# Kernel tuning notes

Hardware: AMD Instinct MI355X
Metric: run time of the kernel (lower is better)

The kernel has to match this reference:

```python
import jax, jax.numpy as jnp
import numpy as np

N = 100000   # nodes
E = 400000   # edges per relation
K = 2        # n_hop relations
D = 256      # in_dim
ATT = 64     # att_dim
L = 3        # n_layer
H1, H2 = 128, 64
EPS = 1e-5
NEG_SLOPE = 0.01


def setup_inputs() -> dict:
    key = jax.random.key(0)
    ks = jax.random.split(key, 16)
    s = 1.0 / np.sqrt(D)
    return {
        "x": jax.random.normal(ks[0], (N, D), jnp.float32),
        "edges_index": jax.random.randint(ks[1], (K, 2, E), 0, N),
        "edges_weight": jax.random.uniform(ks[2], (K, E), jnp.float32),
        "bn_gamma": jnp.ones((D,), jnp.float32),
        "bn_beta": jnp.zeros((D,), jnp.float32),
        "gcn_W": jax.random.normal(ks[3], (L, D, D), jnp.float32) * s,
        "gcn_b": jnp.zeros((L, D), jnp.float32),
        "att_lin_W": jax.random.normal(ks[4], (L, K, D, ATT), jnp.float32) * s,
        "att_lin_b": jnp.zeros((L, K, ATT), jnp.float32),
        "att_q": jax.random.normal(ks[5], (L, K, ATT), jnp.float32) * (1.0 / np.sqrt(ATT)),
        "proj_W1": jax.random.normal(ks[6], (D, H1), jnp.float32) * s,
        "proj_b1": jnp.zeros((H1,), jnp.float32),
        "proj_W2": jax.random.normal(ks[7], (H1, H2), jnp.float32) * (1.0 / np.sqrt(H1)),
        "proj_b2": jnp.zeros((H2,), jnp.float32),
    }


def _gcn_aggregate(row, col, w, xw):
    # symmetric gcn_norm on adj_t (add_self_loops=False):
    # deg[i] = sum of w over edges with col == i
    deg = jax.ops.segment_sum(w, col, num_segments=N)
    dinv = jnp.where(deg > 0, 1.0 / jnp.sqrt(deg), 0.0)
    norm = dinv[col] * w * dinv[row]                       # [E]
    # out[c] += norm * xw[r]
    return jax.ops.segment_sum(norm[:, None] * xw[row], col, num_segments=N)


def reference(x, edges_index, edges_weight, bn_gamma, bn_beta, gcn_W, gcn_b,
              att_lin_W, att_lin_b, att_q, proj_W1, proj_b1, proj_W2, proj_b2):
    # BatchNorm1d (training-mode batch stats)
    mu = jnp.mean(x, axis=0)
    var = jnp.mean((x - mu) ** 2, axis=0)
    h = (x - mu) / jnp.sqrt(var + EPS) * bn_gamma + bn_beta   # [N, D]

    rows = edges_index[:, 0, :]  # [K, E]
    cols = edges_index[:, 1, :]

    for i in range(L):
        xw = h @ gcn_W[i]                                     # shared transform [N, D]
        # per-relation sparse aggregation, vmapped over K
        xs = jax.vmap(_gcn_aggregate, in_axes=(0, 0, 0, None))(
            rows, cols, edges_weight, xw) + gcn_b[i]          # [K, N, D]
        # HanAtt: softmax over hops of per-node scores
        keys = jnp.tanh(jnp.einsum('knd,kdh->knh', xs, att_lin_W[i]) + att_lin_b[i][:, None, :])
        sim = jnp.einsum('knh,kh->kn', keys, att_q[i])        # [K, N]
        alpha = jax.nn.softmax(sim, axis=0)                   # softmax over K
        h = jnp.einsum('knd,kn->nd', xs, alpha)               # [N, D]
        h = jax.nn.relu(h)

    h = jax.nn.leaky_relu(h @ proj_W1 + proj_b1, NEG_SLOPE)
    h = jax.nn.leaky_relu(h @ proj_W2 + proj_b2, NEG_SLOPE)
    return h
```

## Files before the change

kernel.cpp:

```cpp
#include <hip/hip_runtime.h>
#include <hip/hip_bf16.h>
#include <math.h>

#define NN 100000
#define EE 400000
#define KD 2
#define DD 256
#define ATTD 64
#define LL 3
#define HH1 128
#define HH2 64
#define EPSV 1e-5f
#define SLOPE 0.01f
#define KN (KD * NN)
#define WFP 33554432.0f

typedef short short8 __attribute__((ext_vector_type(8)));
typedef float floatx4 __attribute__((ext_vector_type(4)));
typedef unsigned int u32x4 __attribute__((ext_vector_type(4)));
typedef unsigned short u16;
typedef unsigned int u32;
typedef unsigned long long u64;

__device__ __forceinline__ u16 f2bf(float f) {
    u32 u = __float_as_uint(f);
    return (u16)((u + 0x7fffu + ((u >> 16) & 1u)) >> 16);
}
__device__ __forceinline__ float bf2f(u16 h) {
    return __uint_as_float((u32)h << 16);
}

__device__ __forceinline__ void fma_row8_(float4& a0, float4& a1, uint4 w, float nv) {
    float2 f0 = __bfloat1622float2(*(const __hip_bfloat162*)&w.x);
    float2 f1 = __bfloat1622float2(*(const __hip_bfloat162*)&w.y);
    float2 f2 = __bfloat1622float2(*(const __hip_bfloat162*)&w.z);
    float2 f3 = __bfloat1622float2(*(const __hip_bfloat162*)&w.w);
    a0.x += nv * f0.x; a0.y += nv * f0.y; a0.z += nv * f1.x; a0.w += nv * f1.y;
    a1.x += nv * f2.x; a1.y += nv * f2.y; a1.z += nv * f3.x; a1.w += nv * f3.y;
}

__global__ void bn_stats(const float* __restrict__ x, float* __restrict__ sums) {
    int d = threadIdx.x;
    int r0 = blockIdx.x * 125;
    float s = 0.f, sq = 0.f;
    for (int r = r0; r < r0 + 125; ++r) {
        float v = x[(size_t)r * DD + d];
        s += v; sq += v * v;
    }
    atomicAdd(&sums[d], s);
    atomicAdd(&sums[DD + d], sq);
}

__global__ void bn_apply(const float* __restrict__ x, const float* __restrict__ sums,
                         const float* __restrict__ gamma, const float* __restrict__ beta,
                         u16* __restrict__ h_hi, u16* __restrict__ h_lo) {
    size_t i = (size_t)blockIdx.x * blockDim.x + threadIdx.x;
    const float inv_n = 1.f / NN;
    int dq = (int)(i & 63) * 4;
    float4 xv = ((const float4*)x)[i];
    ushort4 hv, lv;
    float* xp = (float*)&xv;
    u16* hp = (u16*)&hv; u16* lp = (u16*)&lv;
#pragma unroll
    for (int j = 0; j < 4; ++j) {
        int d = dq + j;
        float mu = sums[d] * inv_n;
        float var = sums[DD + d] * inv_n - mu * mu;
        float inv = rsqrtf(var + EPSV);
        float v = (xp[j] - mu) * inv * gamma[d] + beta[d];
        u16 hb = f2bf(v);
        hp[j] = hb;
        lp[j] = f2bf(v - bf2f(hb));
    }
    ((ushort4*)h_hi)[i] = hv;
    ((ushort4*)h_lo)[i] = lv;
}

__global__ void deg_count(const int* __restrict__ ei, const float* __restrict__ w,
                          u64* __restrict__ dc) {
    int i = blockIdx.x * blockDim.x + threadIdx.x;
    if (i >= KD * EE) return;
    int k = i / EE, e = i - k * EE;
    int col = ei[(size_t)k * 2 * EE + EE + e];
    u64 wfp = (u64)__float2uint_rn(w[i] * WFP);
    atomicAdd(&dc[k * NN + col], ((u64)1 << 32) | wfp);
}

__global__ void dinv_pack(const u64* __restrict__ dc, float* __restrict__ dinv,
                          int* __restrict__ starts) {
    int i = blockIdx.x * blockDim.x + threadIdx.x;
    if (i >= KN) return;
    u64 p = dc[i];
    float deg = (float)(u32)p * (1.f / WFP);
    dinv[i] = deg > 0.f ? 1.f / sqrtf(deg) : 0.f;
    starts[i] = (int)(p >> 32);
}

#define SCAN_NB ((KN + 255) / 256)
__global__ void scan_blocks(int* __restrict__ starts, int* __restrict__ bsums) {
    __shared__ int tmp[256];
    int t = threadIdx.x;
    int idx = blockIdx.x * 256 + t;
    int v = (idx < KN) ? starts[idx] : 0;
    tmp[t] = v;
    __syncthreads();
#pragma unroll
    for (int off = 1; off < 256; off <<= 1) {
        int s = (t >= off) ? tmp[t - off] : 0;
        __syncthreads();
        tmp[t] += s;
        __syncthreads();
    }
    if (idx < KN) starts[idx] = tmp[t] - v;
    if (t == 255) bsums[blockIdx.x] = tmp[255];
}

__global__ void scan_sums(int* __restrict__ bsums) {
    __shared__ int tmp[1024];
    int t = threadIdx.x;
    int v = (t < SCAN_NB) ? bsums[t] : 0;
    tmp[t] = v;
    __syncthreads();
#pragma unroll
    for (int off = 1; off < 1024; off <<= 1) {
        int s = (t >= off) ? tmp[t - off] : 0;
        __syncthreads();
        tmp[t] += s;
        __syncthreads();
    }
    if (t < SCAN_NB) bsums[t] = tmp[t] - v;
}

__global__ void scan_add(int* __restrict__ starts, const int* __restrict__ bsums) {
    int idx = blockIdx.x * 256 + threadIdx.x;
    if (idx < KN) starts[idx] += bsums[blockIdx.x];
}

__global__ void csr_fill(const int* __restrict__ ei, const float* __restrict__ w,
                         const float* __restrict__ dinv,
                         int* __restrict__ starts, int2* __restrict__ edata) {
    int i = blockIdx.x * blockDim.x + threadIdx.x;
    if (i >= KD * EE) return;
    int k = i / EE, e = i - k * EE;
    const int* eik = ei + (size_t)k * 2 * EE;
    int row = eik[e], col = eik[EE + e];
    float nv = dinv[k * NN + col] * w[i] * dinv[k * NN + row];
    int pos = atomicAdd(&starts[k * NN + col], 1);
    edata[pos] = make_int2(row, __float_as_int(nv));
}

#define GCN_T (LL * DD * DD)
#define ATT_T (LL * KD * DD * ATTD)
#define P1_T  (DD * HH1)
#define P2_T  (HH1 * HH2)
#define WC_TOTAL (GCN_T + ATT_T + P1_T + P2_T)
__device__ __forceinline__ void wconv1(const float* __restrict__ W, u16* __restrict__ Wt,
                                       int i, int Kd, int Nc) {
    int kk = i / Nc, n = i - kk * Nc;
    Wt[(size_t)n * Kd + kk] = f2bf(W[i]);
}
__global__ void wconv_all(const float* __restrict__ gcnW, u16* __restrict__ gcnWb,
                          const float* __restrict__ attW, u16* __restrict__ attWb,
                          const float* __restrict__ pW1, u16* __restrict__ pW1b,
                          const float* __restrict__ pW2, u16* __restrict__ pW2b) {
    int gid = blockIdx.x * 256 + threadIdx.x;
    if (gid >= WC_TOTAL) return;
    if (gid < GCN_T) {
        int l = gid >> 16, i = gid & 65535;
        wconv1(gcnW + (size_t)l * DD * DD, gcnWb + (size_t)l * DD * DD, i, DD, DD);
    } else if (gid < GCN_T + ATT_T) {
        int g = gid - GCN_T;
        int lk = g >> 14, i = g & 16383;
        wconv1(attW + (size_t)lk * DD * ATTD, attWb + (size_t)lk * ATTD * DD, i, DD, ATTD);
    } else if (gid < GCN_T + ATT_T + P1_T) {
        wconv1(pW1, pW1b, gid - (GCN_T + ATT_T), DD, HH1);
    } else {
        wconv1(pW2, pW2b, gid - (GCN_T + ATT_T + P1_T), HH1, HH2);
    }
}

__global__ void att_bias_fold(const float* __restrict__ attW, const float* __restrict__ attb,
                              const float* __restrict__ gcnb, float* __restrict__ batt) {
    int lk = blockIdx.x;
    int a = threadIdx.x;
    int l = lk >> 1;
    const float* W = attW + (size_t)lk * DD * ATTD;
    const float* gb = gcnb + l * DD;
    float s = attb[lk * ATTD + a];
    for (int d = 0; d < DD; ++d) s += gb[d] * W[d * ATTD + a];
    batt[lk * ATTD + a] = s;
}

#define LDSP 40

template<int BN_, int MODE, bool PRESPLIT, bool BIAS, int ACT>
__global__ __launch_bounds__(256) void gemm_mfma(
        const float* __restrict__ A,
        const u16* __restrict__ Ahi, const u16* __restrict__ Alo,
        const u16* __restrict__ Bt, const float* __restrict__ bias,
        float* __restrict__ Cf, u16* __restrict__ Cb,
        int M, int Kd, int Nc) {
    constexpr int JW = BN_ / 64;
    __shared__ u16 AsHi[64 * LDSP];
    __shared__ u16 AsLo[64 * LDSP];
    __shared__ u16 Bs[BN_ * LDSP];

    const int tid = threadIdx.x;
    const int lane = tid & 63, wx = tid >> 6;
    const int lane15 = lane & 15, quad = lane >> 4;
    const int bm = blockIdx.x * 64;
    const int bn = blockIdx.y * BN_;

    floatx4 acc[4][JW];
#pragma unroll
    for (int i = 0; i < 4; ++i)
#pragma unroll
        for (int j = 0; j < JW; ++j) acc[i][j] = (floatx4){0.f, 0.f, 0.f, 0.f};

    for (int k0 = 0; k0 < Kd; k0 += 32) {
        if constexpr (PRESPLIT) {
            {
                int m = tid >> 2, ko = (tid & 3) << 3;
                uint4 vh = make_uint4(0, 0, 0, 0), vl = make_uint4(0, 0, 0, 0);
                if (bm + m < M) {
                    vh = *(const uint4*)(Ahi + (size_t)(bm + m) * Kd + k0 + ko);
                    vl = *(const uint4*)(Alo + (size_t)(bm + m) * Kd + k0 + ko);
                }
                *(uint4*)(void*)(AsHi + m * LDSP + ko) = vh;
                *(uint4*)(void*)(AsLo + m * LDSP + ko) = vl;
            }
        } else {
#pragma unroll
            for (int t = tid; t < 512; t += 256) {
                int m = t >> 3, k4 = (t & 7) << 2;
                float4 v = make_float4(0.f, 0.f, 0.f, 0.f);
                if (bm + m < M) v = *(const float4*)(A + (size_t)(bm + m) * Kd + k0 + k4);
                u16 h0 = f2bf(v.x), h1 = f2bf(v.y), h2 = f2bf(v.z), h3 = f2bf(v.w);
                *(ushort4*)(void*)(AsHi + m * LDSP + k4) = make_ushort4(h0, h1, h2, h3);
                u16 l0 = f2bf(v.x - bf2f(h0)), l1 = f2bf(v.y - bf2f(h1));
                u16 l2 = f2bf(v.z - bf2f(h2)), l3 = f2bf(v.w - bf2f(h3));
                *(ushort4*)(void*)(AsLo + m * LDSP + k4) = make_ushort4(l0, l1, l2, l3);
            }
        }
#pragma unroll
        for (int t = tid; t < BN_ * 4; t += 256) {
            int n = t >> 2, ko = (t & 3) << 3;
            uint4 w = *(const uint4*)(Bt + (size_t)(bn + n) * Kd + k0 + ko);
            *(uint4*)(void*)(Bs + n * LDSP + ko) = w;
        }
        __syncthreads();

        const u16* pA  = AsHi + lane15 * LDSP + quad * 8;
        const u16* pAl = AsLo + lane15 * LDSP + quad * 8;
        const u16* pB  = Bs + (wx * (BN_ / 4) + lane15) * LDSP + quad * 8;
        short8 b[JW];
#pragma unroll
        for (int j = 0; j < JW; ++j) b[j] = *(const short8*)(pB + j * 16 * LDSP);
#pragma unroll
        for (int i = 0; i < 4; ++i) {
            short8 a = *(const short8*)(pA + i * 16 * LDSP);
#pragma unroll
            for (int j = 0; j < JW; ++j)
                acc[i][j] = __builtin_amdgcn_mfma_f32_16x16x32_bf16(a, b[j], acc[i][j], 0, 0, 0);
        }
#pragma unroll
        for (int i = 0; i < 4; ++i) {
            short8 a = *(const short8*)(pAl + i * 16 * LDSP);
#pragma unroll
            for (int j = 0; j < JW; ++j)
                acc[i][j] = __builtin_amdgcn_mfma_f32_16x16x32_bf16(a, b[j], acc[i][j], 0, 0, 0);
        }
        __syncthreads();
    }

#pragma unroll
    for (int i = 0; i < 4; ++i) {
#pragma unroll
        for (int r = 0; r < 4; ++r) {
            int row = bm + i * 16 + quad * 4 + r;
            if (row >= M) continue;
#pragma unroll
            for (int j = 0; j < JW; ++j) {
                int col = bn + wx * (BN_ / 4) + j * 16 + lane15;
                float v = acc[i][j][r];
                if constexpr (BIAS) v += bias[col];
                if constexpr (ACT == 1) v = v > 0.f ? v : SLOPE * v;
                if constexpr (MODE == 0) Cf[(size_t)row * Nc + col] = v;
                else                     Cb[(size_t)row * Nc + col] = f2bf(v);
            }
        }
    }
}

#define BMF 32
#define ALDS 264

__global__ __launch_bounds__(256) void att_fused(
        const int* __restrict__ starts, const int2* __restrict__ edata,
        const u16* __restrict__ xw, const u16* __restrict__ Bt,
        const float* __restrict__ batt, const float* __restrict__ qv,
        const float* __restrict__ gcnb,
        u16* __restrict__ h_hi, u16* __restrict__ h_lo) {
    __shared__ u16 As[KD * BMF * ALDS];
    __shared__ float simbuf[KD][2][BMF];

    const int tid = threadIdx.x;
    const int lane = tid & 63, waveid = tid >> 6;
    const int l32 = tid & 31;
    const int hid = tid >> 5;
    const int base = lane & 32;
    const int bm = blockIdx.x * BMF;

    {
        const int kk = hid >> 2;
        const int r0 = (hid & 3) * 8;
        const int widx0 = kk * NN + bm + r0;
        int sv = 0;
        if (l32 < 9) {
            int idx = widx0 - 1 + l32;
            sv = idx >= 0 ? starts[idx] : 0;
        }
        int2 ed[8];
#pragma unroll
        for (int g = 0; g < 8; ++g) {
            int b = __shfl(sv, base + g), e = __shfl(sv, base + g + 1);
            ed[g] = (l32 < e - b) ? edata[b + l32] : make_int2(0, 0);
        }
#pragma unroll
        for (int g = 0; g < 8; g += 2) {
            int bA = __shfl(sv, base + g),     eA = __shfl(sv, base + g + 1);
            int eB = __shfl(sv, base + g + 2);
            int bB = eA;
            int dA = eA - bA, dB = eB - bB;
            int mA = dA > 32 ? 32 : dA, mB = dB > 32 ? 32 : dB;
            float4 xa0 = make_float4(0.f,0.f,0.f,0.f), xa1 = make_float4(0.f,0.f,0.f,0.f);
            float4 xb0 = make_float4(0.f,0.f,0.f,0.f), xb1 = make_float4(0.f,0.f,0.f,0.f);
            int j = 0;
            for (; j + 4 <= mA && j + 4 <= mB; j += 4) {
                int ra0 = __shfl(ed[g].x, base + j),     ra1 = __shfl(ed[g].x, base + j + 1);
                int ra2 = __shfl(ed[g].x, base + j + 2), ra3 = __shfl(ed[g].x, base + j + 3);
                int rb0 = __shfl(ed[g+1].x, base + j),     rb1 = __shfl(ed[g+1].x, base + j + 1);
                int rb2 = __shfl(ed[g+1].x, base + j + 2), rb3 = __shfl(ed[g+1].x, base + j + 3);
                float na0 = __int_as_float(__shfl(ed[g].y, base + j));
                float na1 = __int_as_float(__shfl(ed[g].y, base + j + 1));
                float na2 = __int_as_float(__shfl(ed[g].y, base + j + 2));
                float na3 = __int_as_float(__shfl(ed[g].y, base + j + 3));
                float nb0 = __int_as_float(__shfl(ed[g+1].y, base + j));
                float nb1 = __int_as_float(__shfl(ed[g+1].y, base + j + 1));
                float nb2 = __int_as_float(__shfl(ed[g+1].y, base + j + 2));
                float nb3 = __int_as_float(__shfl(ed[g+1].y, base + j + 3));
                uint4 wa0 = *(const uint4*)(xw + (size_t)ra0 * DD + l32 * 8);
                uint4 wa1 = *(const uint4*)(xw + (size_t)ra1 * DD + l32 * 8);
                uint4 wa2 = *(const uint4*)(xw + (size_t)ra2 * DD + l32 * 8);
                uint4 wa3 = *(const uint4*)(xw + (size_t)ra3 * DD + l32 * 8);
                uint4 wb0 = *(const uint4*)(xw + (size_t)rb0 * DD + l32 * 8);
                uint4 wb1 = *(const uint4*)(xw + (size_t)rb1 * DD + l32 * 8);
                uint4 wb2 = *(const uint4*)(xw + (size_t)rb2 * DD + l32 * 8);
                uint4 wb3 = *(const uint4*)(xw + (size_t)rb3 * DD + l32 * 8);
                fma_row8_(xa0, xa1, wa0, na0);
                fma_row8_(xa0, xa1, wa1, na1);
                fma_row8_(xa0, xa1, wa2, na2);
                fma_row8_(xa0, xa1, wa3, na3);
                fma_row8_(xb0, xb1, wb0, nb0);
                fma_row8_(xb0, xb1, wb1, nb1);
                fma_row8_(xb0, xb1, wb2, nb2);
                fma_row8_(xb0, xb1, wb3, nb3);
            }
            int jb = j;
            for (; j + 4 <= mA; j += 4) {
                int ra0 = __shfl(ed[g].x, base + j),     ra1 = __shfl(ed[g].x, base + j + 1);
                int ra2 = __shfl(ed[g].x, base + j + 2), ra3 = __shfl(ed[g].x, base + j + 3);
                float na0 = __int_as_float(__shfl(ed[g].y, base + j));
                float na1 = __int_as_float(__shfl(ed[g].y, base + j + 1));
                float na2 = __int_as_float(__shfl(ed[g].y, base + j + 2));
                float na3 = __int_as_float(__shfl(ed[g].y, base + j + 3));
                uint4 wa0 = *(const uint4*)(xw + (size_t)ra0 * DD + l32 * 8);
                uint4 wa1 = *(const uint4*)(xw + (size_t)ra1 * DD + l32 * 8);
                uint4 wa2 = *(const uint4*)(xw + (size_t)ra2 * DD + l32 * 8);
                uint4 wa3 = *(const uint4*)(xw + (size_t)ra3 * DD + l32 * 8);
                fma_row8_(xa0, xa1, wa0, na0);
                fma_row8_(xa0, xa1, wa1, na1);
                fma_row8_(xa0, xa1, wa2, na2);
                fma_row8_(xa0, xa1, wa3, na3);
            }
            for (; j < mA; ++j) {
                int r = __shfl(ed[g].x, base + j);
                float nv = __int_as_float(__shfl(ed[g].y, base + j));
                uint4 w = *(const uint4*)(xw + (size_t)r * DD + l32 * 8);
                fma_row8_(xa0, xa1, w, nv);
            }
            for (; jb + 4 <= mB; jb += 4) {
                int rb0 = __shfl(ed[g+1].x, base + jb),     rb1 = __shfl(ed[g+1].x, base + jb + 1);
                int rb2 = __shfl(ed[g+1].x, base + jb + 2), rb3 = __shfl(ed[g+1].x, base + jb + 3);
                float nb0 = __int_as_float(__shfl(ed[g+1].y, base + jb));
                float nb1 = __int_as_float(__shfl(ed[g+1].y, base + jb + 1));
                float nb2 = __int_as_float(__shfl(ed[g+1].y, base + jb + 2));
                float nb3 = __int_as_float(__shfl(ed[g+1].y, base + jb + 3));
                uint4 wb0 = *(const uint4*)(xw + (size_t)rb0 * DD + l32 * 8);
                uint4 wb1 = *(const uint4*)(xw + (size_t)rb1 * DD + l32 * 8);
                uint4 wb2 = *(const uint4*)(xw + (size_t)rb2 * DD + l32 * 8);
                uint4 wb3 = *(const uint4*)(xw + (size_t)rb3 * DD + l32 * 8);
                fma_row8_(xb0, xb1, wb0, nb0);
                fma_row8_(xb0, xb1, wb1, nb1);
                fma_row8_(xb0, xb1, wb2, nb2);
                fma_row8_(xb0, xb1, wb3, nb3);
            }
            for (; jb < mB; ++jb) {
                int r = __shfl(ed[g+1].x, base + jb);
                float nv = __int_as_float(__shfl(ed[g+1].y, base + jb));
                uint4 w = *(const uint4*)(xw + (size_t)r * DD + l32 * 8);
                fma_row8_(xb0, xb1, w, nv);
            }
            for (int e2 = bA + 32; e2 < eA; ++e2) {
                int2 ee = edata[e2];
                float nv = __int_as_float(ee.y);
                uint4 w = *(const uint4*)(xw + (size_t)ee.x * DD + l32 * 8);
                fma_row8_(xa0, xa1, w, nv);
            }
            for (int e2 = bB + 32; e2 < eB; ++e2) {
                int2 ee = edata[e2];
                float nv = __int_as_float(ee.y);
                uint4 w = *(const uint4*)(xw + (size_t)ee.x * DD + l32 * 8);
                fma_row8_(xb0, xb1, w, nv);
            }
            u32x4 st;
            st.x = (u32)f2bf(xa0.x) | ((u32)f2bf(xa0.y) << 16);
            st.y = (u32)f2bf(xa0.z) | ((u32)f2bf(xa0.w) << 16);
            st.z = (u32)f2bf(xa1.x) | ((u32)f2bf(xa1.y) << 16);
            st.w = (u32)f2bf(xa1.z) | ((u32)f2bf(xa1.w) << 16);
            *(u32x4*)(void*)(As + (kk * BMF + r0 + g) * ALDS + l32 * 8) = st;
            st.x = (u32)f2bf(xb0.x) | ((u32)f2bf(xb0.y) << 16);
            st.y = (u32)f2bf(xb0.z) | ((u32)f2bf(xb0.w) << 16);
            st.z = (u32)f2bf(xb1.x) | ((u32)f2bf(xb1.y) << 16);
            st.w = (u32)f2bf(xb1.z) | ((u32)f2bf(xb1.w) << 16);
            *(u32x4*)(void*)(As + (kk * BMF + r0 + g + 1) * ALDS + l32 * 8) = st;
        }
    }
    __syncthreads();

    const int kw = waveid >> 1, ch = waveid & 1;
    const int lane15 = lane & 15, quad = lane >> 4;
    floatx4 acc[2][2];
#pragma unroll
    for (int i = 0; i < 2; ++i)
#pragma unroll
        for (int j = 0; j < 2; ++j) acc[i][j] = (floatx4){0.f, 0.f, 0.f, 0.f};

    const u16* pB0 = Bt + (size_t)kw * ATTD * DD + (size_t)(ch * 32 + lane15) * DD + quad * 8;
    const u16* pB1 = pB0 + 16 * DD;
#pragma unroll
    for (int k0 = 0; k0 < DD; k0 += 32) {
        short8 b0 = *(const short8*)(pB0 + k0);
        short8 b1 = *(const short8*)(pB1 + k0);
        const u16* pA = As + (kw * BMF + lane15) * ALDS + k0 + quad * 8;
#pragma unroll
        for (int i = 0; i < 2; ++i) {
            short8 a = *(const short8*)(pA + i * 16 * ALDS);
            acc[i][0] = __builtin_amdgcn_mfma_f32_16x16x32_bf16(a, b0, acc[i][0], 0, 0, 0);
            acc[i][1] = __builtin_amdgcn_mfma_f32_16x16x32_bf16(a, b1, acc[i][1], 0, 0, 0);
        }
    }

#pragma unroll
    for (int i = 0; i < 2; ++i) {
#pragma unroll
        for (int r = 0; r < 4; ++r) {
            float p = 0.f;
#pragma unroll
            for (int j = 0; j < 2; ++j) {
                int col = ch * 32 + j * 16 + lane15;
                float v = acc[i][j][r] + batt[kw * ATTD + col];
                float ex = __expf(2.f * v);
                float th = 1.f - 2.f / (ex + 1.f);
                p += th * qv[kw * ATTD + col];
            }
            p += __shfl_xor(p, 1, 64);
            p += __shfl_xor(p, 2, 64);
            p += __shfl_xor(p, 4, 64);
            p += __shfl_xor(p, 8, 64);
            if (lane15 == 0) simbuf[kw][ch][i * 16 + quad * 4 + r] = p;
        }
    }
    __syncthreads();

#pragma unroll
    for (int it = 0; it < 4; ++it) {
        int item = tid + it * 256;
        int row = item >> 5, c8 = item & 31;
        int grow = bm + row;
        float s0 = simbuf[0][0][row] + simbuf[0][1][row];
        float s1 = simbuf[1][0][row] + simbuf[1][1][row];
        float m = fmaxf(s0, s1);
        float e0 = __expf(s0 - m), e1 = __expf(s1 - m);
        float inv = 1.f / (e0 + e1);
        float a0 = e0 * inv, a1 = e1 * inv;
        uint4 x0 = *(const uint4*)(As + row * ALDS + c8 * 8);
        uint4 x1 = *(const uint4*)(As + (BMF + row) * ALDS + c8 * 8);
        const float* bp = gcnb + c8 * 8;
        uint4 hiw, low;
        u16* hp = (u16*)&hiw; u16* lp = (u16*)&low;
        const u32* xp0 = (const u32*)&x0; const u32* xp1 = (const u32*)&x1;
#pragma unroll
        for (int j = 0; j < 4; ++j) {
            float2 f0 = __bfloat1622float2(*(const __hip_bfloat162*)&xp0[j]);
            float2 f1 = __bfloat1622float2(*(const __hip_bfloat162*)&xp1[j]);
            float ra = fmaxf(0.f, a0 * f0.x + a1 * f1.x + bp[2 * j]);
            float rb = fmaxf(0.f, a0 * f0.y + a1 * f1.y + bp[2 * j + 1]);
            u16 ha = f2bf(ra), hb = f2bf(rb);
            hp[2 * j] = ha; hp[2 * j + 1] = hb;
            lp[2 * j] = f2bf(ra - bf2f(ha));
            lp[2 * j + 1] = f2bf(rb - bf2f(hb));
        }
        *(uint4*)(h_hi + (size_t)grow * DD + c8 * 8) = hiw;
        *(uint4*)(h_lo + (size_t)grow * DD + c8 * 8) = low;
    }
}

extern "C" void kernel_launch(void* const* d_in, const int* in_sizes, int n_in,
                              void* d_out, int out_size, void* d_ws, size_t ws_size,
                              hipStream_t stream) {
    const float* x     = (const float*)d_in[0];
    const int*   ei    = (const int*)d_in[1];
    const float* ew    = (const float*)d_in[2];
    const float* gamma = (const float*)d_in[3];
    const float* beta  = (const float*)d_in[4];
    const float* gcn_W = (const float*)d_in[5];
    const float* gcn_b = (const float*)d_in[6];
    const float* att_W = (const float*)d_in[7];
    const float* att_b = (const float*)d_in[8];
    const float* att_q = (const float*)d_in[9];
    const float* pW1   = (const float*)d_in[10];
    const float* pb1   = (const float*)d_in[11];
    const float* pW2   = (const float*)d_in[12];
    const float* pb2   = (const float*)d_in[13];
    float* out = (float*)d_out;

    char* wsb = (char*)d_ws;
    size_t off = 0;
    auto alloc = [&](size_t bytes) -> void* {
        void* p = wsb + off;
        off += (bytes + 255) & ~(size_t)255;
        return p;
    };
    u16*   h_hi  = (u16*)alloc((size_t)NN * DD * 2);
    u16*   h_lo  = (u16*)alloc((size_t)NN * DD * 2);
    u16*   xw    = (u16*)alloc((size_t)NN * DD * 2);
    float* p1tmp = (float*)xw;
    float* dinv  = (float*)alloc((size_t)KN * 4);
    int*   starts= (int*)alloc(((size_t)KN + 1) * 4);
    u64*   dc    = (u64*)alloc((size_t)KN * 8);
    int2*  edata = (int2*)alloc((size_t)KD * EE * 8);
    float* bnsums= (float*)alloc(2 * DD * 4);
    u16*   gcnWb = (u16*)alloc((size_t)LL * DD * DD * 2);
    u16*   attWb = (u16*)alloc((size_t)LL * KD * ATTD * DD * 2);
    u16*   pW1b  = (u16*)alloc((size_t)HH1 * DD * 2);
    u16*   pW2b  = (u16*)alloc((size_t)HH2 * HH1 * 2);
    float* batt  = (float*)alloc((size_t)LL * KD * ATTD * 4);
    int*   bsums = (int*)alloc((size_t)SCAN_NB * 4);

    wconv_all<<<(WC_TOTAL + 255) / 256, 256, 0, stream>>>(
        gcn_W, gcnWb, att_W, attWb, pW1, pW1b, pW2, pW2b);
    att_bias_fold<<<LL * KD, ATTD, 0, stream>>>(att_W, att_b, gcn_b, batt);

    hipMemsetAsync(bnsums, 0, 2 * DD * 4, stream);
    bn_stats<<<800, 256, 0, stream>>>(x, bnsums);
    bn_apply<<<25000, 256, 0, stream>>>(x, bnsums, gamma, beta, h_hi, h_lo);

    hipMemsetAsync(dc, 0, (size_t)KN * 8, stream);
    deg_count<<<(KD * EE + 255) / 256, 256, 0, stream>>>(ei, ew, dc);
    dinv_pack<<<(KN + 255) / 256, 256, 0, stream>>>(dc, dinv, starts);
    scan_blocks<<<SCAN_NB, 256, 0, stream>>>(starts, bsums);
    scan_sums<<<1, 1024, 0, stream>>>(bsums);
    scan_add<<<SCAN_NB, 256, 0, stream>>>(starts, bsums);
    csr_fill<<<(KD * EE + 255) / 256, 256, 0, stream>>>(ei, ew, dinv, starts, edata);

    const int MB64 = (NN + 63) / 64;
    const int MBF  = NN / BMF;
    for (int l = 0; l < LL; ++l) {
        gemm_mfma<256, 1, true, false, 0><<<dim3(MB64, 1), 256, 0, stream>>>(
            nullptr, h_hi, h_lo, gcnWb + (size_t)l * DD * DD, nullptr,
            nullptr, xw, NN, DD, DD);
        att_fused<<<MBF, 256, 0, stream>>>(
            starts, edata, xw, attWb + (size_t)l * KD * ATTD * DD,
            batt + (size_t)l * KD * ATTD, att_q + (size_t)l * KD * ATTD,
            gcn_b + l * DD, h_hi, h_lo);
    }

    gemm_mfma<128, 0, true, true, 1><<<dim3(MB64, 1), 256, 0, stream>>>(
        nullptr, h_hi, h_lo, pW1b, pb1, p1tmp, nullptr, NN, DD, HH1);
    gemm_mfma<64, 0, false, true, 1><<<dim3(MB64, 1), 256, 0, stream>>>(
        p1tmp, nullptr, nullptr, pW2b, pb2, out, nullptr, NN, HH1, HH2);
}
```

Baseline: 904.7 us.

## Fuse next layer's GCN weight GEMM into attention aggregation kernel epilogue

For the first two layers, the fused aggregation/attention kernel now keeps the post-ReLU h tile (hi/lo bf16 split) in shared memory. It multiplies that tile by the next layer's GCN weight with MFMA and writes xw directly into a ping-pong buffer. This removes two standalone GEMM launches and the global write and re-read of h_hi/h_lo between layers. In exchange, each 32-row block re-reads the full 256x256 weight from global/L2, adds register pressure, and writes xw with scalar 2-byte stores.

```diff
diff --git a/kernel.cpp b/kernel.cpp
--- a/kernel.cpp
+++ b/kernel.cpp
@@ -295,11 +295,13 @@
 #define BMF 32
 #define ALDS 264
 
+template<bool LAST>
 __global__ __launch_bounds__(256) void att_fused(
         const int* __restrict__ starts, const int2* __restrict__ edata,
         const u16* __restrict__ xw, const u16* __restrict__ Bt,
         const float* __restrict__ batt, const float* __restrict__ qv,
         const float* __restrict__ gcnb,
+        const u16* __restrict__ Wnext, u16* __restrict__ xwout,
         u16* __restrict__ h_hi, u16* __restrict__ h_lo) {
     __shared__ u16 As[KD * BMF * ALDS];
     __shared__ float simbuf[KD][2][BMF];
@@ -314,7 +316,8 @@
     {
         const int kk = hid >> 2;
         const int r0 = (hid & 3) * 8;
-        const int widx0 = kk * NN + bm + r0;
+        const int widx0 = kk * NN + bm + (hid & 3) * 8;
+        (void)r0;
         int sv = 0;
         if (l32 < 9) {
             int idx = widx0 - 1 + l32;
@@ -423,17 +426,19 @@
                 uint4 w = *(const uint4*)(xw + (size_t)ee.x * DD + l32 * 8);
                 fma_row8_(xb0, xb1, w, nv);
             }
+            const int kk2 = hid >> 2;
+            const int rr = (hid & 3) * 8;
             u32x4 st;
             st.x = (u32)f2bf(xa0.x) | ((u32)f2bf(xa0.y) << 16);
             st.y = (u32)f2bf(xa0.z) | ((u32)f2bf(xa0.w) << 16);
             st.z = (u32)f2bf(xa1.x) | ((u32)f2bf(xa1.y) << 16);
             st.w = (u32)f2bf(xa1.z) | ((u32)f2bf(xa1.w) << 16);
-            *(u32x4*)(void*)(As + (kk * BMF + r0 + g) * ALDS + l32 * 8) = st;
+            *(u32x4*)(void*)(As + (kk2 * BMF + rr + g) * ALDS + l32 * 8) = st;
             st.x = (u32)f2bf(xb0.x) | ((u32)f2bf(xb0.y) << 16);
             st.y = (u32)f2bf(xb0.z) | ((u32)f2bf(xb0.w) << 16);
             st.z = (u32)f2bf(xb1.x) | ((u32)f2bf(xb1.y) << 16);
             st.w = (u32)f2bf(xb1.z) | ((u32)f2bf(xb1.w) << 16);
-            *(u32x4*)(void*)(As + (kk * BMF + r0 + g + 1) * ALDS + l32 * 8) = st;
+            *(u32x4*)(void*)(As + (kk2 * BMF + rr + g + 1) * ALDS + l32 * 8) = st;
         }
     }
     __syncthreads();
@@ -483,11 +488,11 @@
     }
     __syncthreads();
 
+    uint4 hw[4], lw[4];
 #pragma unroll
     for (int it = 0; it < 4; ++it) {
         int item = tid + it * 256;
         int row = item >> 5, c8 = item & 31;
-        int grow = bm + row;
         float s0 = simbuf[0][0][row] + simbuf[0][1][row];
         float s1 = simbuf[1][0][row] + simbuf[1][1][row];
         float m = fmaxf(s0, s1);
@@ -497,8 +502,7 @@
         uint4 x0 = *(const uint4*)(As + row * ALDS + c8 * 8);
         uint4 x1 = *(const uint4*)(As + (BMF + row) * ALDS + c8 * 8);
         const float* bp = gcnb + c8 * 8;
-        uint4 hiw, low;
-        u16* hp = (u16*)&hiw; u16* lp = (u16*)&low;
+        u16* hp = (u16*)&hw[it]; u16* lp = (u16*)&lw[it];
         const u32* xp0 = (const u32*)&x0; const u32* xp1 = (const u32*)&x1;
 #pragma unroll
         for (int j = 0; j < 4; ++j) {
@@ -511,8 +515,63 @@
             lp[2 * j] = f2bf(ra - bf2f(ha));
             lp[2 * j + 1] = f2bf(rb - bf2f(hb));
         }
-        *(uint4*)(h_hi + (size_t)grow * DD + c8 * 8) = hiw;
-        *(uint4*)(h_lo + (size_t)grow * DD + c8 * 8) = low;
+    }
+
+    if constexpr (LAST) {
+#pragma unroll
+        for (int it = 0; it < 4; ++it) {
+            int item = tid + it * 256;
+            int row = item >> 5, c8 = item & 31;
+            size_t off = (size_t)(bm + row) * DD + c8 * 8;
+            *(uint4*)(h_hi + off) = hw[it];
+            *(uint4*)(h_lo + off) = lw[it];
+        }
+    } else {
+        __syncthreads();
+#pragma unroll
+        for (int it = 0; it < 4; ++it) {
+            int item = tid + it * 256;
+            int row = item >> 5, c8 = item & 31;
+            *(uint4*)(void*)(As + row * ALDS + c8 * 8) = hw[it];
+            *(uint4*)(void*)(As + (BMF + row) * ALDS + c8 * 8) = lw[it];
+        }
+        __syncthreads();
+
+        const int wx = waveid;
+        floatx4 acc2[2][4];
+#pragma unroll
+        for (int i = 0; i < 2; ++i)
+#pragma unroll
+            for (int j = 0; j < 4; ++j) acc2[i][j] = (floatx4){0.f, 0.f, 0.f, 0.f};
+
+#pragma unroll
+        for (int k0 = 0; k0 < DD; k0 += 32) {
+            short8 b[4];
+#pragma unroll
+            for (int j = 0; j < 4; ++j)
+                b[j] = *(const short8*)(Wnext + (size_t)(wx * 64 + j * 16 + lane15) * DD + k0 + quad * 8);
+#pragma unroll
+            for (int i = 0; i < 2; ++i) {
+                short8 ahi = *(const short8*)(As + (i * 16 + lane15) * ALDS + k0 + quad * 8);
+                short8 alo = *(const short8*)(As + (BMF + i * 16 + lane15) * ALDS + k0 + quad * 8);
+#pragma unroll
+                for (int j = 0; j < 4; ++j) {
+                    acc2[i][j] = __builtin_amdgcn_mfma_f32_16x16x32_bf16(ahi, b[j], acc2[i][j], 0, 0, 0);
+                    acc2[i][j] = __builtin_amdgcn_mfma_f32_16x16x32_bf16(alo, b[j], acc2[i][j], 0, 0, 0);
+                }
+            }
+        }
+#pragma unroll
+        for (int i = 0; i < 2; ++i)
+#pragma unroll
+            for (int r = 0; r < 4; ++r) {
+                int row = bm + i * 16 + quad * 4 + r;
+#pragma unroll
+                for (int j = 0; j < 4; ++j) {
+                    int col = wx * 64 + j * 16 + lane15;
+                    xwout[(size_t)row * DD + col] = f2bf(acc2[i][j][r]);
+                }
+            }
     }
 }
 
@@ -544,8 +603,9 @@
     };
     u16*   h_hi  = (u16*)alloc((size_t)NN * DD * 2);
     u16*   h_lo  = (u16*)alloc((size_t)NN * DD * 2);
-    u16*   xw    = (u16*)alloc((size_t)NN * DD * 2);
-    float* p1tmp = (float*)xw;
+    u16*   xw_a  = (u16*)alloc((size_t)NN * DD * 2);
+    u16*   xw_b  = (u16*)alloc((size_t)NN * DD * 2);
+    float* p1tmp = (float*)xw_b;
     float* dinv  = (float*)alloc((size_t)KN * 4);
     int*   starts= (int*)alloc(((size_t)KN + 1) * 4);
     u64*   dc    = (u64*)alloc((size_t)KN * 8);
@@ -576,15 +636,24 @@
 
     const int MB64 = (NN + 63) / 64;
     const int MBF  = NN / BMF;
-    for (int l = 0; l < LL; ++l) {
-        gemm_mfma<256, 1, true, false, 0><<<dim3(MB64, 1), 256, 0, stream>>>(
-            nullptr, h_hi, h_lo, gcnWb + (size_t)l * DD * DD, nullptr,
-            nullptr, xw, NN, DD, DD);
-        att_fused<<<MBF, 256, 0, stream>>>(
-            starts, edata, xw, attWb + (size_t)l * KD * ATTD * DD,
-            batt + (size_t)l * KD * ATTD, att_q + (size_t)l * KD * ATTD,
-            gcn_b + l * DD, h_hi, h_lo);
-    }
+
+    gemm_mfma<256, 1, true, false, 0><<<dim3(MB64, 1), 256, 0, stream>>>(
+        nullptr, h_hi, h_lo, gcnWb, nullptr, nullptr, xw_a, NN, DD, DD);
+
+    att_fused<false><<<MBF, 256, 0, stream>>>(
+        starts, edata, xw_a, attWb + (size_t)0 * KD * ATTD * DD,
+        batt + 0 * KD * ATTD, att_q + 0 * KD * ATTD, gcn_b + 0 * DD,
+        gcnWb + (size_t)1 * DD * DD, xw_b, nullptr, nullptr);
+
+    att_fused<false><<<MBF, 256, 0, stream>>>(
+        starts, edata, xw_b, attWb + (size_t)1 * KD * ATTD * DD,
+        batt + 1 * KD * ATTD, att_q + 1 * KD * ATTD, gcn_b + 1 * DD,
+        gcnWb + (size_t)2 * DD * DD, xw_a, nullptr, nullptr);
+
+    att_fused<true><<<MBF, 256, 0, stream>>>(
+        starts, edata, xw_a, attWb + (size_t)2 * KD * ATTD * DD,
+        batt + 2 * KD * ATTD, att_q + 2 * KD * ATTD, gcn_b + 2 * DD,
+        nullptr, nullptr, h_hi, h_lo);
 
     gemm_mfma<128, 0, true, true, 1><<<dim3(MB64, 1), 256, 0, stream>>>(
         nullptr, h_hi, h_lo, pW1b, pb1, p1tmp, nullptr, NN, DD, HH1);
```

Result: faster. 844.7 us (-6.6%).
